# Kernel optimization log

Hardware: AMD Instinct MI355X
Metric: run time of the kernel (lower is better)

The kernel has to match this reference:

```python
import jax, jax.numpy as jnp
import numpy as np

EPSILON = 1e-05


def setup_inputs() -> dict:
    key = jax.random.key(0)
    k1, k2, k3 = jax.random.split(key, 3)
    B, T, D, K = 8, 4096, 256, 2048
    hidden_states = jax.random.normal(k1, (B, T, D), dtype=jnp.float32)
    embed_sum = jax.random.normal(k2, (K, D), dtype=jnp.float32)
    # cluster usage counts are positive in practice
    cluster_usage = jax.random.uniform(k3, (K,), dtype=jnp.float32) * 10.0 + 0.1
    return {
        "hidden_states": hidden_states,
        "embed_sum": embed_sum,
        "cluster_usage": cluster_usage,
    }


def reference(hidden_states, embed_sum, cluster_usage):
    # embed = embed_sum / clamp(cluster_usage, eps)   -> [K, D]
    embed = embed_sum / jnp.clip(cluster_usage, EPSILON, None)[:, None]

    shape = hidden_states.shape
    x = hidden_states.reshape(-1, shape[-1])  # [N, D]

    # squared L2 distances via norm expansion (argmin equals argmin of cdist p=2)
    x_sq = jnp.sum(x * x, axis=-1, keepdims=True)          # [N, 1]
    e_sq = jnp.sum(embed * embed, axis=-1)[None, :]         # [1, K]
    dots = jnp.einsum("nd,kd->nk", x, embed)               # [N, K]
    dists = x_sq - 2.0 * dots + e_sq                        # [N, K]

    embed_ind = jnp.argmin(dists, axis=-1)                 # [N]
    embed_ind = embed_ind.reshape(shape[:-1])              # [B, T]

    # decode: embedding lookup
    quantize = embed[embed_ind]                             # [B, T, D]
    return quantize, embed_ind
```

## Files before the change

kernel.cpp:

```cpp
#include <hip/hip_runtime.h>
#include <float.h>
#include <stdint.h>


#define EPSILON 1e-5f
#define DELTA   1e-3f

constexpr int D     = 256;
constexpr int K_TOT = 2048;

constexpr int RES_H      = 16384;
constexpr int ESQ_H      = 32768;
constexpr int LDS_HALVES = 36864;
constexpr int DYN_LDS    = LDS_HALVES * 2;

typedef _Float16 half8v  __attribute__((ext_vector_type(8)));
typedef _Float16 half4v  __attribute__((ext_vector_type(4)));
typedef float    f32x4   __attribute__((ext_vector_type(4)));

#define GLL(SRC, DST)                                                   \
  __builtin_amdgcn_global_load_lds(                                     \
      (const __attribute__((address_space(1))) void*)(SRC),             \
      (__attribute__((address_space(3))) void*)(DST), 16, 0, 0)

__global__ void prep_kernel(const float* __restrict__ es,
                            const float* __restrict__ usage,
                            _Float16* __restrict__ ec,
                            float* __restrict__ esq,
                            int* __restrict__ counter) {
  const int bx   = blockIdx.x;
  const int t    = threadIdx.x;
  const int wid  = t >> 6;
  const int lane = t & 63;
  if (bx < K_TOT / 4) {
    const int k = bx * 4 + wid;
    const float u = fmaxf(usage[k], EPSILON);
    const float4 v = *(const float4*)(es + (size_t)k * D + lane * 4);
    float4 e;
    e.x = v.x / u; e.y = v.y / u; e.z = v.z / u; e.w = v.w / u;
    half4v h, lo;
    h.x = (_Float16)e.x; lo.x = (_Float16)(e.x - (float)h.x);
    h.y = (_Float16)e.y; lo.y = (_Float16)(e.y - (float)h.y);
    h.z = (_Float16)e.z; lo.z = (_Float16)(e.z - (float)h.z);
    h.w = (_Float16)e.w; lo.w = (_Float16)(e.w - (float)h.w);
    *(half4v*)(ec + (size_t)k * 512 + lane * 4)       = h;
    *(half4v*)(ec + (size_t)k * 512 + 256 + lane * 4) = lo;
    float s = e.x * e.x + e.y * e.y + e.z * e.z + e.w * e.w;
    #pragma unroll
    for (int m = 1; m < 64; m <<= 1) s += __shfl_xor(s, m, 64);
    if (lane == 0) esq[k] = s;
  } else {
    if (t == 0) *counter = 0;
  }
}

__global__ __launch_bounds__(256, 2)
void mm_kernel(const float* __restrict__ x, const _Float16* __restrict__ ec,
               const float* __restrict__ esq, const float* __restrict__ es,
               const float* __restrict__ usage,
               float* __restrict__ out_q, float* __restrict__ out_i,
               int* __restrict__ list, int* __restrict__ counter,
               unsigned long long* __restrict__ rmin,
               int* __restrict__ tick, int N) {
  extern __shared__ __align__(16) _Float16 lds[];
  const int t    = threadIdx.x;
  const int lane = t & 63;
  const int q    = lane >> 4;
  const int l15  = lane & 15;
  const int wid  = t >> 6;
  const int wn   = wid >> 1;
  const int wk   = wid & 1;
  const int n0   = blockIdx.x * 64;

  float* esq_lds = (float*)&lds[ESQ_H];
  {
    *(float4*)&esq_lds[t * 8]     = *(const float4*)(esq + t * 8);
    *(float4*)&esq_lds[t * 8 + 4] = *(const float4*)(esq + t * 8 + 4);
  }

  const int prow  = t >> 2;
  const int pc    = t & 3;
  const int wbase = (t >> 6) * 512 + ((t & 63) ^ ((t >> 3) & 3)) * 8;
  #pragma unroll
  for (int i = 0; i < 8; ++i) {
    const float* src = x + (size_t)(n0 + prow) * D + i * 32 + pc * 8;
    const float4 f0 = *(const float4*)src;
    const float4 f1 = *(const float4*)(src + 4);
    const float f[8] = {f0.x, f0.y, f0.z, f0.w, f1.x, f1.y, f1.z, f1.w};
    half8v hv, lv;
    #pragma unroll
    for (int e = 0; e < 8; ++e) {
      const _Float16 h = (_Float16)f[e];
      hv[e] = h;
      lv[e] = (_Float16)(f[e] - (float)h);
    }
    *(half8v*)&lds[i * 2048 + wbase]         = hv;
    *(half8v*)&lds[RES_H + i * 2048 + wbase] = lv;
  }
  __syncthreads();

  const int gA = l15 * 4 + q;
  const int sp = (gA ^ ((l15 >> 1) & 3)) * 8;

  half8v ahr[8][2];
  #pragma unroll
  for (int s = 0; s < 8; ++s)
    #pragma unroll
    for (int mi = 0; mi < 2; ++mi)
      ahr[s][mi] = *(const half8v*)
          &lds[s * 2048 + (wn * 2 + mi) * 512 + sp];
  __syncthreads();

  const int r0 = t >> 3;
  const int cl = (t & 7) ^ (r0 & 7);
  const _Float16* pB = ec + (size_t)r0 * 512 + cl * 8;

  #pragma unroll
  for (int i = 0; i < 4; ++i)
    GLL(pB + i * 16384, &lds[i * 2048 + t * 8]);

  int bfoff[4][2];
  #pragma unroll
  for (int ni = 0; ni < 4; ++ni)
    #pragma unroll
    for (int j = 0; j < 2; ++j)
      bfoff[ni][j] = (wk * 64 + ni * 16 + l15) * 64 +
                     (((j << 2) + q) ^ (l15 & 7)) * 8;

  float rd0[2][4], rd1[2][4];
  int   ri0[2][4];
  #pragma unroll
  for (int mi = 0; mi < 2; ++mi)
    #pragma unroll
    for (int r = 0; r < 4; ++r) {
      rd0[mi][r] = FLT_MAX; rd1[mi][r] = FLT_MAX; ri0[mi][r] = 0x7fffffff;
    }

  for (int kt = 0; kt < 16; ++kt) {
    int   kc[4];
    float eqv[4];
    #pragma unroll
    for (int ni = 0; ni < 4; ++ni) {
      kc[ni]  = kt * 128 + wk * 64 + ni * 16 + l15;
      eqv[ni] = esq_lds[kc[ni]];
    }

    f32x4 acc[2][4] = {};

    #pragma unroll
    for (int sidx = 0; sidx < 8; ++sidx) {
      const int ss = kt * 8 + sidx;
      asm volatile("s_waitcnt vmcnt(0)" ::: "memory");
      __builtin_amdgcn_s_barrier();
      __builtin_amdgcn_sched_barrier(0);

      if (ss < 127) {
        const int ns = ss + 1;
        const _Float16* np = pB + (size_t)(ns >> 3) * 65536 + (ns & 7) * 64;
        const int nb = (ns & 1) * 8192;
        #pragma unroll
        for (int i = 0; i < 4; ++i)
          GLL(np + i * 16384, &lds[nb + i * 2048 + t * 8]);
      }

      const int bb = (ss & 1) * 8192;
      __builtin_amdgcn_s_setprio(1);
      #pragma unroll
      for (int j = 0; j < 2; ++j) {
        half8v bf[4];
        #pragma unroll
        for (int ni = 0; ni < 4; ++ni)
          bf[ni] = *(const half8v*)&lds[bb + bfoff[ni][j]];
        const int ks = (sidx & 3) * 2 + j;
        if (sidx < 4) {
          half8v al[2];
          #pragma unroll
          for (int mi = 0; mi < 2; ++mi)
            al[mi] = *(const half8v*)
                &lds[RES_H + ks * 2048 + (wn * 2 + mi) * 512 + sp];
          #pragma unroll
          for (int mi = 0; mi < 2; ++mi)
            #pragma unroll
            for (int ni = 0; ni < 4; ++ni)
              acc[mi][ni] = __builtin_amdgcn_mfma_f32_16x16x32_f16(
                  ahr[ks][mi], bf[ni], acc[mi][ni], 0, 0, 0);
          #pragma unroll
          for (int mi = 0; mi < 2; ++mi)
            #pragma unroll
            for (int ni = 0; ni < 4; ++ni)
              acc[mi][ni] = __builtin_amdgcn_mfma_f32_16x16x32_f16(
                  al[mi], bf[ni], acc[mi][ni], 0, 0, 0);
        } else {
          #pragma unroll
          for (int mi = 0; mi < 2; ++mi)
            #pragma unroll
            for (int ni = 0; ni < 4; ++ni)
              acc[mi][ni] = __builtin_amdgcn_mfma_f32_16x16x32_f16(
                  ahr[ks][mi], bf[ni], acc[mi][ni], 0, 0, 0);
        }
      }
      __builtin_amdgcn_s_setprio(0);
    }

    #pragma unroll
    for (int ni = 0; ni < 4; ++ni) {
      #pragma unroll
      for (int mi = 0; mi < 2; ++mi) {
        #pragma unroll
        for (int r = 0; r < 4; ++r) {
          const float d = fmaf(-2.f, acc[mi][ni][r], eqv[ni]);
          if (d < rd0[mi][r]) {
            rd1[mi][r] = rd0[mi][r]; rd0[mi][r] = d; ri0[mi][r] = kc[ni];
          } else {
            rd1[mi][r] = fminf(rd1[mi][r], d);
          }
        }
      }
    }
  }
  __syncthreads();

  float* ex = (float*)lds;
  #pragma unroll
  for (int mi = 0; mi < 2; ++mi) {
    #pragma unroll
    for (int r = 0; r < 4; ++r) {
      float d0 = rd0[mi][r], d1 = rd1[mi][r];
      int   i0 = ri0[mi][r];
      #pragma unroll
      for (int off = 1; off < 16; off <<= 1) {
        const float od0 = __shfl_xor(d0, off, 16);
        const int   oi0 = __shfl_xor(i0, off, 16);
        const float od1 = __shfl_xor(d1, off, 16);
        if (od0 < d0 || (od0 == d0 && oi0 < i0)) {
          d1 = fminf(d0, od1); d0 = od0; i0 = oi0;
        } else {
          d1 = fminf(d1, od0);
        }
      }
      if (l15 == mi * 8 + r) {
        const int row = wn * 32 + mi * 16 + q * 4 + r;
        *(float4*)&ex[(row * 2 + wk) * 4] =
            make_float4(d0, __int_as_float(i0), d1, 0.f);
      }
    }
  }
  __syncthreads();

  {
    const int row = t >> 2;
    const int seg = t & 3;
    const float4 a = *(const float4*)&ex[(row * 2 + 0) * 4];
    const float4 b = *(const float4*)&ex[(row * 2 + 1) * 4];
    float d0, d1; int i0;
    const int ia = __float_as_int(a.y), ib = __float_as_int(b.y);
    if (b.x < a.x || (b.x == a.x && ib < ia)) {
      d0 = b.x; i0 = ib; d1 = fminf(a.x, b.z);
    } else {
      d0 = a.x; i0 = ia; d1 = fminf(a.z, b.x);
    }
    const int n = n0 + row;
    const float u  = fmaxf(usage[i0], EPSILON);
    const float4* src = (const float4*)(es + (size_t)i0 * D);
    float4*       dst = (float4*)(out_q + (size_t)n * D);
    #pragma unroll
    for (int i = 0; i < 16; ++i) {
      const int j = i * 4 + seg;
      const float4 e = src[j];
      dst[j] = make_float4(e.x / u, e.y / u, e.z / u, e.w / u);
    }
    if (seg == 0) {
      out_i[n] = (float)i0;
      if (d1 - d0 < DELTA) {
        rmin[n] = 0xFFFFFFFFFFFFFFFFull;
        tick[n] = 0;
        const int pos = atomicAdd(counter, 1);
        list[pos] = n;
      }
    }
  }
}

__global__ void repair_kernel(const float* __restrict__ x,
                              const float* __restrict__ es,
                              const float* __restrict__ usage,
                              const float* __restrict__ esq,
                              const int* __restrict__ list,
                              const int* __restrict__ counter,
                              unsigned long long* __restrict__ rmin,
                              int* __restrict__ tick,
                              float* __restrict__ out_q,
                              float* __restrict__ out_i) {
  __shared__ float xs[256];
  const int t    = threadIdx.x;
  const int w    = t >> 6;
  const int lane = t & 63;
  const int cnt  = *counter;
  const int kseg = blockIdx.x & 7;

  for (int j = blockIdx.x >> 3; j < cnt; j += 256) {
    const int n = list[j];
    __syncthreads();
    xs[t] = x[(size_t)n * D + t];
    __syncthreads();
    const float4 xv = *(const float4*)&xs[lane * 4];

    float bd = FLT_MAX;
    int   bi = 0x7fffffff;
    const int kb0 = kseg * 256 + w * 64;
    for (int kk = 0; kk < 64; kk += 4) {
      const int kbase = kb0 + kk;
      float pd[4];
      #pragma unroll
      for (int j2 = 0; j2 < 4; ++j2) {
        const int k = kbase + j2;
        const float rs = 1.0f / fmaxf(usage[k], EPSILON);
        const float4 e = *(const float4*)(es + (size_t)k * D + lane * 4);
        float p = xv.x * (e.x * rs);
        p = fmaf(xv.y, e.y * rs, p);
        p = fmaf(xv.z, e.z * rs, p);
        pd[j2] = fmaf(xv.w, e.w * rs, p);
      }
      #pragma unroll
      for (int off = 1; off < 64; off <<= 1) {
        pd[0] += __shfl_xor(pd[0], off, 64);
        pd[1] += __shfl_xor(pd[1], off, 64);
        pd[2] += __shfl_xor(pd[2], off, 64);
        pd[3] += __shfl_xor(pd[3], off, 64);
      }
      #pragma unroll
      for (int j2 = 0; j2 < 4; ++j2) {
        const float dst = fmaf(-2.f, pd[j2], esq[kbase + j2]);
        if (dst < bd) { bd = dst; bi = kbase + j2; }
      }
    }
    int widx = -1;
    if (lane == 0) {
      uint32_t ub = __float_as_uint(bd);
      ub = (ub & 0x80000000u) ? ~ub : (ub | 0x80000000u);
      const unsigned long long pk =
          ((unsigned long long)ub << 32) | (unsigned)bi;
      atomicMin(&rmin[n], pk);
      __threadfence();
      const int done = atomicAdd(&tick[n], 1);
      if (done == 31) {
        __threadfence();
        const unsigned long long fin = atomicAdd(&rmin[n], 0ull);
        widx = (int)(fin & 0x7fffffffu);
      }
    }
    widx = __shfl(widx, 0, 64);
    if (widx >= 0) {
      const float u = fmaxf(usage[widx], EPSILON);
      const float4 e = *(const float4*)(es + (size_t)widx * D + lane * 4);
      *(float4*)(out_q + (size_t)n * D + lane * 4) =
          make_float4(e.x / u, e.y / u, e.z / u, e.w / u);
      if (lane == 0) out_i[n] = (float)widx;
    }
  }
}

constexpr int TN = 128;
constexpr int DC = 32;
constexpr int KS = 2;
constexpr int RS = 196;

__global__ void esq_kernel(const float* __restrict__ es,
                           const float* __restrict__ usage,
                           float* __restrict__ esq) {
  const int lane = threadIdx.x & 63;
  const int w    = threadIdx.x >> 6;
  const int k    = blockIdx.x * 4 + w;
  const float u  = fmaxf(usage[k], EPSILON);
  const float4 e = *(const float4*)(es + (size_t)k * D + lane * 4);
  const float a = e.x / u, b = e.y / u, c = e.z / u, d = e.w / u;
  float s = a * a + b * b + c * c + d * d;
  #pragma unroll
  for (int m = 1; m < 64; m <<= 1) s += __shfl_xor(s, m, 64);
  if (lane == 0) esq[k] = s;
}

__global__ __launch_bounds__(256, 2)
void dist_kernel(const float* __restrict__ x,
                 const float* __restrict__ es,
                 const float* __restrict__ usage,
                 const float* __restrict__ esq,
                 float* __restrict__ bestd,
                 int* __restrict__ besti, int N) {
  __shared__ float smX[DC * RS];
  __shared__ float smE[DC * RS];
  const int t    = threadIdx.x;
  const int tx   = t & 15;
  const int ty   = t >> 4;
  const int n0   = blockIdx.x * TN;
  const int half = blockIdx.y;

  float best[8];
  int   bidx[8];
  #pragma unroll
  for (int i = 0; i < 8; ++i) { best[i] = FLT_MAX; bidx[i] = 0; }

  for (int kt = 0; kt < (K_TOT / KS) / 128; ++kt) {
    const int k0 = half * (K_TOT / KS) + kt * 128;
    float acc[8][8];
    #pragma unroll
    for (int i = 0; i < 8; ++i)
      #pragma unroll
      for (int j = 0; j < 8; ++j) acc[i][j] = 0.f;

    for (int dc = 0; dc < D; dc += DC) {
      __syncthreads();
      #pragma unroll
      for (int i = 0; i < 4; ++i) {
        const int f    = i * 256 + t;
        const int row  = f >> 3;
        const int c4   = f & 7;
        const int pcol = row + ((row >> 3) << 2);
        const float4 xv =
            *(const float4*)(x + (size_t)(n0 + row) * D + dc + c4 * 4);
        smX[(c4 * 4 + 0) * RS + pcol] = xv.x;
        smX[(c4 * 4 + 1) * RS + pcol] = xv.y;
        smX[(c4 * 4 + 2) * RS + pcol] = xv.z;
        smX[(c4 * 4 + 3) * RS + pcol] = xv.w;
        const int kk = k0 + row;
        const float rs = 1.0f / fmaxf(usage[kk], EPSILON);
        const float4 ev =
            *(const float4*)(es + (size_t)kk * D + dc + c4 * 4);
        smE[(c4 * 4 + 0) * RS + pcol] = ev.x * rs;
        smE[(c4 * 4 + 1) * RS + pcol] = ev.y * rs;
        smE[(c4 * 4 + 2) * RS + pcol] = ev.z * rs;
        smE[(c4 * 4 + 3) * RS + pcol] = ev.w * rs;
      }
      __syncthreads();
      #pragma unroll 4
      for (int d = 0; d < DC; ++d) {
        const float* px = &smX[d * RS + ty * 12];
        const float* pe = &smE[d * RS + tx * 12];
        const float4 xa = *(const float4*)px;
        const float4 xb = *(const float4*)(px + 4);
        const float4 ea = *(const float4*)pe;
        const float4 eb = *(const float4*)(pe + 4);
        const float xr[8] = {xa.x, xa.y, xa.z, xa.w, xb.x, xb.y, xb.z, xb.w};
        const float er[8] = {ea.x, ea.y, ea.z, ea.w, eb.x, eb.y, eb.z, eb.w};
        #pragma unroll
        for (int i = 0; i < 8; ++i)
          #pragma unroll
          for (int jj = 0; jj < 8; ++jj)
            acc[i][jj] = fmaf(xr[i], er[jj], acc[i][jj]);
      }
    }
    #pragma unroll
    for (int jj = 0; jj < 8; ++jj) {
      const int k = k0 + tx * 8 + jj;
      const float eq = esq[k];
      #pragma unroll
      for (int i = 0; i < 8; ++i) {
        const float dst = fmaf(-2.0f, acc[i][jj], eq);
        if (dst < best[i]) { best[i] = dst; bidx[i] = k; }
      }
    }
  }
  __syncthreads();
  float* rd = smX;
  int*   ri = (int*)smE;
  #pragma unroll
  for (int i = 0; i < 8; ++i) {
    const int r = ty * 8 + i;
    rd[tx * TN + r] = best[i];
    ri[tx * TN + r] = bidx[i];
  }
  __syncthreads();
  for (int off = 8; off >= 1; off >>= 1) {
    if (tx < off) {
      #pragma unroll
      for (int i = 0; i < 8; ++i) {
        const int r = ty * 8 + i;
        const float da = rd[tx * TN + r], db = rd[(tx + off) * TN + r];
        const int   ia = ri[tx * TN + r], ib = ri[(tx + off) * TN + r];
        if (db < da || (db == da && ib < ia)) {
          rd[tx * TN + r] = db;
          ri[tx * TN + r] = ib;
        }
      }
    }
    __syncthreads();
  }
  if (tx == 0) {
    #pragma unroll
    for (int i = 0; i < 8; ++i) {
      const int r = ty * 8 + i;
      bestd[(size_t)half * N + n0 + r] = rd[r];
      besti[(size_t)half * N + n0 + r] = ri[r];
    }
  }
}

__global__ void gather_kernel(const float* __restrict__ es,
                              const float* __restrict__ usage,
                              const float* __restrict__ bestd,
                              const int* __restrict__ besti,
                              float* __restrict__ out_q,
                              float* __restrict__ out_i, int N) {
  const int w    = threadIdx.x >> 6;
  const int lane = threadIdx.x & 63;
  const int n    = blockIdx.x * 4 + w;
  const float d0 = bestd[n];
  const float d1 = bestd[(size_t)N + n];
  const int   i0 = besti[n];
  const int   i1 = besti[(size_t)N + n];
  const int idx = (d1 < d0) ? i1 : i0;
  const float u = fmaxf(usage[idx], EPSILON);
  const float4 e = *(const float4*)(es + (size_t)idx * D + lane * 4);
  float4 qv;
  qv.x = e.x / u; qv.y = e.y / u; qv.z = e.z / u; qv.w = e.w / u;
  *(float4*)(out_q + (size_t)n * D + lane * 4) = qv;
  if (lane == 0) out_i[n] = (float)idx;
}

extern "C" void kernel_launch(void* const* d_in, const int* in_sizes, int n_in,
                              void* d_out, int out_size, void* d_ws, size_t ws_size,
                              hipStream_t stream) {
  const float* x     = (const float*)d_in[0];
  const float* es    = (const float*)d_in[1];
  const float* usage = (const float*)d_in[2];
  const int N = in_sizes[0] / D;

  float* out_q = (float*)d_out;
  float* out_i = out_q + (size_t)N * D;

  const size_t EB = (size_t)K_TOT * 512 * 2;
  const size_t off_esq  = EB;
  const size_t off_list = off_esq + 8192;
  const size_t off_cnt  = off_list + (size_t)N * 4;
  const size_t off_rmin = off_cnt + 16;
  const size_t off_tick = off_rmin + (size_t)N * 8;
  const size_t NEED     = off_tick + (size_t)N * 4;

  char* wsb = (char*)d_ws;

  hipError_t attr_ok = hipFuncSetAttribute(
      (const void*)mm_kernel, hipFuncAttributeMaxDynamicSharedMemorySize,
      DYN_LDS);

  if (ws_size >= NEED && attr_ok == hipSuccess && (N % 64) == 0) {
    _Float16* ec   = (_Float16*)wsb;
    float*    esq  = (float*)(wsb + off_esq);
    int*      list = (int*)(wsb + off_list);
    int*      cnt  = (int*)(wsb + off_cnt);
    unsigned long long* rmin = (unsigned long long*)(wsb + off_rmin);
    int*      tick = (int*)(wsb + off_tick);

    prep_kernel<<<K_TOT / 4 + 1, 256, 0, stream>>>(es, usage, ec, esq, cnt);
    mm_kernel<<<N / 64, 256, DYN_LDS, stream>>>(x, ec, esq, es, usage,
                                                out_q, out_i, list, cnt,
                                                rmin, tick, N);
    repair_kernel<<<2048, 256, 0, stream>>>(x, es, usage, esq, list, cnt,
                                            rmin, tick, out_q, out_i);
  } else {
    float* ws    = (float*)d_ws;
    float* esq   = ws;
    float* bestd = ws + K_TOT;
    int*   besti = (int*)(ws + K_TOT + (size_t)KS * N);
    esq_kernel<<<K_TOT / 4, 256, 0, stream>>>(es, usage, esq);
    dist_kernel<<<dim3(N / TN, KS), 256, 0, stream>>>(x, es, usage, esq,
                                                      bestd, besti, N);
    gather_kernel<<<N / 4, 256, 0, stream>>>(es, usage, bestd, besti,
                                             out_q, out_i, N);
  }
}
```

Baseline: 202.4 us.

## Double the mm_kernel row tile to 128 and use a 4-stage B ring buffer

Each mm_kernel block now has 512 threads and covers 128 query rows instead of 64. Each codebook tile loaded into LDS is therefore shared by twice as many waves, which halves global/L2 traffic for the codebook per row. The B prefetch becomes a 4-slot ring that loads two k-stages per barrier, cutting barrier and waitcnt overhead. In exchange, LDS use grows to about 139 KB per block, which likely allows only one block per CU. There are also fewer, larger blocks, which could hurt load balance and latency hiding.

```diff
diff --git a/kernel.cpp b/kernel.cpp
--- a/kernel.cpp
+++ b/kernel.cpp
@@ -9,9 +9,9 @@
 constexpr int D     = 256;
 constexpr int K_TOT = 2048;
 
-constexpr int RES_H      = 16384;
-constexpr int ESQ_H      = 32768;
-constexpr int LDS_HALVES = 36864;
+constexpr int RES_H      = 32768;
+constexpr int ESQ_H      = 65536;
+constexpr int LDS_HALVES = 69632;
 constexpr int DYN_LDS    = LDS_HALVES * 2;
 
 typedef _Float16 half8v  __attribute__((ext_vector_type(8)));
@@ -54,7 +54,7 @@
   }
 }
 
-__global__ __launch_bounds__(256, 2)
+__global__ __launch_bounds__(512, 2)
 void mm_kernel(const float* __restrict__ x, const _Float16* __restrict__ ec,
                const float* __restrict__ esq, const float* __restrict__ es,
                const float* __restrict__ usage,
@@ -70,12 +70,12 @@
   const int wid  = t >> 6;
   const int wn   = wid >> 1;
   const int wk   = wid & 1;
-  const int n0   = blockIdx.x * 64;
+  const int n0   = blockIdx.x * 128;
 
   float* esq_lds = (float*)&lds[ESQ_H];
   {
-    *(float4*)&esq_lds[t * 8]     = *(const float4*)(esq + t * 8);
-    *(float4*)&esq_lds[t * 8 + 4] = *(const float4*)(esq + t * 8 + 4);
+    const float4 ev = *(const float4*)(esq + t * 4);
+    *(float4*)&esq_lds[t * 4] = ev;
   }
 
   const int prow  = t >> 2;
@@ -94,8 +94,8 @@
       hv[e] = h;
       lv[e] = (_Float16)(f[e] - (float)h);
     }
-    *(half8v*)&lds[i * 2048 + wbase]         = hv;
-    *(half8v*)&lds[RES_H + i * 2048 + wbase] = lv;
+    *(half8v*)&lds[i * 4096 + wbase]         = hv;
+    *(half8v*)&lds[RES_H + i * 4096 + wbase] = lv;
   }
   __syncthreads();
 
@@ -107,8 +107,7 @@
   for (int s = 0; s < 8; ++s)
     #pragma unroll
     for (int mi = 0; mi < 2; ++mi)
-      ahr[s][mi] = *(const half8v*)
-          &lds[s * 2048 + (wn * 2 + mi) * 512 + sp];
+      ahr[s][mi] = *(const half8v*)&lds[s * 4096 + wn * 1024 + mi * 512 + sp];
   __syncthreads();
 
   const int r0 = t >> 3;
@@ -116,8 +115,11 @@
   const _Float16* pB = ec + (size_t)r0 * 512 + cl * 8;
 
   #pragma unroll
-  for (int i = 0; i < 4; ++i)
-    GLL(pB + i * 16384, &lds[i * 2048 + t * 8]);
+  for (int s = 0; s < 2; ++s) {
+    const _Float16* sp0 = pB + s * 64;
+    GLL(sp0,         &lds[s * 8192 + t * 8]);
+    GLL(sp0 + 32768, &lds[s * 8192 + 4096 + t * 8]);
+  }
 
   int bfoff[4][2];
   #pragma unroll
@@ -148,55 +150,62 @@
     f32x4 acc[2][4] = {};
 
     #pragma unroll
-    for (int sidx = 0; sidx < 8; ++sidx) {
-      const int ss = kt * 8 + sidx;
+    for (int hv2 = 0; hv2 < 4; ++hv2) {
+      const int ivl = kt * 4 + hv2;
       asm volatile("s_waitcnt vmcnt(0)" ::: "memory");
       __builtin_amdgcn_s_barrier();
       __builtin_amdgcn_sched_barrier(0);
 
-      if (ss < 127) {
-        const int ns = ss + 1;
-        const _Float16* np = pB + (size_t)(ns >> 3) * 65536 + (ns & 7) * 64;
-        const int nb = (ns & 1) * 8192;
+      if (ivl < 63) {
         #pragma unroll
-        for (int i = 0; i < 4; ++i)
-          GLL(np + i * 16384, &lds[nb + i * 2048 + t * 8]);
-      }
-
-      const int bb = (ss & 1) * 8192;
+        for (int u = 0; u < 2; ++u) {
+          const int ns = ivl * 2 + 2 + u;
+          const _Float16* np = pB + (size_t)(ns >> 3) * 65536 + (ns & 7) * 64;
+          const int nb = (ns & 3) * 8192;
+          GLL(np,         &lds[nb + t * 8]);
+          GLL(np + 32768, &lds[nb + 4096 + t * 8]);
+        }
+      }
+
       __builtin_amdgcn_s_setprio(1);
       #pragma unroll
-      for (int j = 0; j < 2; ++j) {
-        half8v bf[4];
+      for (int u = 0; u < 2; ++u) {
+        const int sidx = hv2 * 2 + u;
+        const int ss   = kt * 8 + sidx;
+        const int bb   = (ss & 3) * 8192;
         #pragma unroll
-        for (int ni = 0; ni < 4; ++ni)
-          bf[ni] = *(const half8v*)&lds[bb + bfoff[ni][j]];
-        const int ks = (sidx & 3) * 2 + j;
-        if (sidx < 4) {
-          half8v al[2];
+        for (int j = 0; j < 2; ++j) {
+          half8v bf[4];
           #pragma unroll
-          for (int mi = 0; mi < 2; ++mi)
-            al[mi] = *(const half8v*)
-                &lds[RES_H + ks * 2048 + (wn * 2 + mi) * 512 + sp];
-          #pragma unroll
-          for (int mi = 0; mi < 2; ++mi)
+          for (int ni = 0; ni < 4; ++ni)
+            bf[ni] = *(const half8v*)&lds[bb + bfoff[ni][j]];
+          const int ks = (sidx & 3) * 2 + j;
+          if (sidx < 4) {
+            half8v al[2];
             #pragma unroll
-            for (int ni = 0; ni < 4; ++ni)
-              acc[mi][ni] = __builtin_amdgcn_mfma_f32_16x16x32_f16(
-                  ahr[ks][mi], bf[ni], acc[mi][ni], 0, 0, 0);
-          #pragma unroll
-          for (int mi = 0; mi < 2; ++mi)
+            for (int mi = 0; mi < 2; ++mi)
+              al[mi] = *(const half8v*)
+                  &lds[RES_H + ks * 4096 + wn * 1024 + mi * 512 + sp];
             #pragma unroll
-            for (int ni = 0; ni < 4; ++ni)
-              acc[mi][ni] = __builtin_amdgcn_mfma_f32_16x16x32_f16(
-                  al[mi], bf[ni], acc[mi][ni], 0, 0, 0);
-        } else {
-          #pragma unroll
-          for (int mi = 0; mi < 2; ++mi)
+            for (int mi = 0; mi < 2; ++mi)
+              #pragma unroll
+              for (int ni = 0; ni < 4; ++ni)
+                acc[mi][ni] = __builtin_amdgcn_mfma_f32_16x16x32_f16(
+                    ahr[ks][mi], bf[ni], acc[mi][ni], 0, 0, 0);
             #pragma unroll
-            for (int ni = 0; ni < 4; ++ni)
-              acc[mi][ni] = __builtin_amdgcn_mfma_f32_16x16x32_f16(
-                  ahr[ks][mi], bf[ni], acc[mi][ni], 0, 0, 0);
+            for (int mi = 0; mi < 2; ++mi)
+              #pragma unroll
+              for (int ni = 0; ni < 4; ++ni)
+                acc[mi][ni] = __builtin_amdgcn_mfma_f32_16x16x32_f16(
+                    al[mi], bf[ni], acc[mi][ni], 0, 0, 0);
+          } else {
+            #pragma unroll
+            for (int mi = 0; mi < 2; ++mi)
+              #pragma unroll
+              for (int ni = 0; ni < 4; ++ni)
+                acc[mi][ni] = __builtin_amdgcn_mfma_f32_16x16x32_f16(
+                    ahr[ks][mi], bf[ni], acc[mi][ni], 0, 0, 0);
+          }
         }
       }
       __builtin_amdgcn_s_setprio(0);
@@ -542,7 +551,7 @@
       (const void*)mm_kernel, hipFuncAttributeMaxDynamicSharedMemorySize,
       DYN_LDS);
 
-  if (ws_size >= NEED && attr_ok == hipSuccess && (N % 64) == 0) {
+  if (ws_size >= NEED && attr_ok == hipSuccess && (N % 128) == 0) {
     _Float16* ec   = (_Float16*)wsb;
     float*    esq  = (float*)(wsb + off_esq);
     int*      list = (int*)(wsb + off_list);
@@ -551,9 +560,9 @@
     int*      tick = (int*)(wsb + off_tick);
 
     prep_kernel<<<K_TOT / 4 + 1, 256, 0, stream>>>(es, usage, ec, esq, cnt);
-    mm_kernel<<<N / 64, 256, DYN_LDS, stream>>>(x, ec, esq, es, usage,
-                                                out_q, out_i, list, cnt,
-                                                rmin, tick, N);
+    mm_kernel<<<N / 128, 512, DYN_LDS, stream>>>(x, ec, esq, es, usage,
+                                                 out_q, out_i, list, cnt,
+                                                 rmin, tick, N);
     repair_kernel<<<2048, 256, 0, stream>>>(x, es, usage, esq, list, cnt,
                                             rmin, tick, out_q, out_i);
   } else {
```

Measured after the change: 196.8 us. 1.03x faster.
